# Performance work log

Measured on AMD Instinct MI355X. Metric: run time of the kernel, lower is better.

Reference implementation:

```python
import jax, jax.numpy as jnp
import numpy as np

B = 8; C = 128; EXP = 4; H = 112; W = 112; K = 3; PAD = 1; STRIDE = 1
IN_C = C * EXP  # 512
EPS = 1e-5


def setup_inputs() -> dict:
    key = jax.random.key(0)
    ks = jax.random.split(key, 24)
    f32 = jnp.float32

    def n(k, shape, s=0.05):
        return jax.random.normal(k, shape, f32) * s

    def bn_params(k):
        k1, k2, k3, k4 = jax.random.split(k, 4)
        g = 1.0 + 0.1 * jax.random.normal(k1, (), f32)  # placeholder, per-channel below
        return k1, k2, k3, k4

    inp = {}
    inp["x"] = jax.random.normal(ks[0], (B, IN_C, H, W), f32)
    # conv1: 1x1, 512 -> 128
    inp["w1"] = n(ks[1], (C, IN_C))
    inp["b1"] = n(ks[2], (C,))
    # bn1
    inp["g1"] = 1.0 + 0.1 * jax.random.normal(ks[3], (C,), f32)
    inp["be1"] = 0.1 * jax.random.normal(ks[4], (C,), f32)
    inp["m1"] = 0.1 * jax.random.normal(ks[5], (C,), f32)
    inp["v1"] = 1.0 + 0.1 * jax.random.uniform(ks[6], (C,), f32)
    # offset conv: 3x3, C -> 18 (small weights so sampling offsets stay modest)
    inp["woff"] = n(ks[7], (2 * K * K, C, K, K), 0.01)
    inp["boff"] = jnp.zeros((2 * K * K,), f32)
    # deformable conv weight: 3x3, C -> C
    inp["wd"] = n(ks[8], (C, C, K, K))
    inp["bd"] = n(ks[9], (C,))
    # bn2
    inp["g2"] = 1.0 + 0.1 * jax.random.normal(ks[10], (C,), f32)
    inp["be2"] = 0.1 * jax.random.normal(ks[11], (C,), f32)
    inp["m2"] = 0.1 * jax.random.normal(ks[12], (C,), f32)
    inp["v2"] = 1.0 + 0.1 * jax.random.uniform(ks[13], (C,), f32)
    # conv2: 1x1, 128 -> 512
    inp["w2"] = n(ks[14], (IN_C, C))
    inp["b2"] = n(ks[15], (IN_C,))
    # bn3
    inp["g3"] = 1.0 + 0.1 * jax.random.normal(ks[16], (IN_C,), f32)
    inp["be3"] = 0.1 * jax.random.normal(ks[17], (IN_C,), f32)
    inp["m3"] = 0.1 * jax.random.normal(ks[18], (IN_C,), f32)
    inp["v3"] = 1.0 + 0.1 * jax.random.uniform(ks[19], (IN_C,), f32)
    return inp


def conv1x1(x, w, b):
    return jnp.einsum("oc,bchw->bohw", w, x) + b[None, :, None, None]


def bn(x, g, be, m, v):
    inv = g / jnp.sqrt(v + EPS)
    return x * inv[None, :, None, None] + (be - m * inv)[None, :, None, None]


def conv3x3(x, w, b):
    out = jax.lax.conv_general_dilated(
        x, w, (STRIDE, STRIDE), ((PAD, PAD), (PAD, PAD)),
        dimension_numbers=("NCHW", "OIHW", "NCHW"))
    return out + b[None, :, None, None]


def deform_conv(x, offset, w, b):
    # x: [B, Cin, H, W]; offset: [B, 2*K*K, Ho, Wo] (y,x interleaved per kernel pt)
    Bn, Cin, Hh, Ww = x.shape
    Ho, Wo = offset.shape[2], offset.shape[3]
    P = Ho * Wo
    off = offset.reshape(Bn, K * K, 2, Ho, Wo)
    kk = jnp.arange(K * K)
    ky = (kk // K).astype(jnp.float32)  # 0..2
    kx = (kk % K).astype(jnp.float32)
    base_y = jnp.arange(Ho, dtype=jnp.float32) * STRIDE - PAD
    base_x = jnp.arange(Wo, dtype=jnp.float32) * STRIDE - PAD
    py = base_y[None, None, :, None] + ky[None, :, None, None] + off[:, :, 0]  # [B,9,Ho,Wo]
    px = base_x[None, None, None, :] + kx[None, :, None, None] + off[:, :, 1]
    y0 = jnp.floor(py); x0 = jnp.floor(px)
    dy = (py - y0).reshape(Bn, 1, -1)  # [B,1,9*P]
    dx = (px - x0).reshape(Bn, 1, -1)
    x_flat = x.reshape(Bn, Cin, Hh * Ww)

    def gather(yi, xi):
        valid = ((yi >= 0) & (yi <= Hh - 1) & (xi >= 0) & (xi <= Ww - 1))
        yc = jnp.clip(yi, 0, Hh - 1).astype(jnp.int32)
        xc = jnp.clip(xi, 0, Ww - 1).astype(jnp.int32)
        idx = (yc * Ww + xc).reshape(Bn, -1)  # [B, 9*P]
        g = jax.vmap(lambda xb, ib: xb[:, ib])(x_flat, idx)  # [B, Cin, 9*P]
        return g * valid.reshape(Bn, 1, -1).astype(x.dtype)

    v00 = gather(y0, x0)
    v01 = gather(y0, x0 + 1)
    v10 = gather(y0 + 1, x0)
    v11 = gather(y0 + 1, x0 + 1)
    cols = (v00 * (1 - dy) * (1 - dx) + v01 * (1 - dy) * dx
            + v10 * dy * (1 - dx) + v11 * dy * dx)  # [B, Cin, 9*P]
    cols = cols.reshape(Bn, Cin * K * K, P)
    out = jnp.einsum("oi,bip->bop", w.reshape(w.shape[0], -1), cols)
    out = out + b[None, :, None]
    return out.reshape(Bn, w.shape[0], Ho, Wo)


def reference(x, w1, b1, g1, be1, m1, v1, woff, boff, wd, bd,
              g2, be2, m2, v2, w2, b2, g3, be3, m3, v3):
    out = jax.nn.relu(bn(conv1x1(x, w1, b1), g1, be1, m1, v1))
    offset = conv3x3(out, woff, boff)
    out = deform_conv(out, offset, wd, bd)
    out = bn(out, g2, be2, m2, v2)
    out = bn(conv1x1(out, w2, b2), g3, be3, m3, v3)
    return jax.nn.relu(out + x)
```

## Files before the change

### kernel.cpp

```cpp
#include <hip/hip_runtime.h>
#include <hip/hip_bf16.h>


typedef __attribute__((ext_vector_type(8))) short short8;
typedef __attribute__((ext_vector_type(4))) float f32x4;

constexpr int Bn = 8;
constexpr int IC = 512;
constexpr int Cc = 128;
constexpr int Hh = 112;
constexpr int Ww = 112;
constexpr int Pp = Hh * Ww;
constexpr float EPSf = 1e-5f;

constexpr size_t OFS_OFFS  = 0;
constexpr size_t OFS_OUT2B = 2097152;
constexpr size_t OFS_W1B   = (size_t)Bn * Pp * IC / 2;
constexpr size_t OFS_W2B   = OFS_W1B + (size_t)Cc * IC / 2;
constexpr size_t OFS_WDB   = OFS_W2B + (size_t)IC * Cc / 2;
constexpr size_t OFS_WOFB  = OFS_WDB + (size_t)9 * Cc * Cc / 2;

__device__ __forceinline__ ushort f2bf(float f) {
  uint u = __float_as_uint(f);
  return (ushort)((u + 0x7fffu + ((u >> 16) & 1u)) >> 16);
}
__device__ __forceinline__ float bfLO(uint u) {
  return __uint_as_float(u << 16);
}
__device__ __forceinline__ float bfHI(uint u) {
  return __uint_as_float(u & 0xffff0000u);
}
__device__ __forceinline__ uint cvtpk(float a, float b) {
  __hip_bfloat162 h = __float22bfloat162_rn(make_float2(a, b));
  return *(uint*)&h;
}

__global__ __launch_bounds__(256) void prep_kernel(
    const float* __restrict__ w1, const float* __restrict__ w2,
    const float* __restrict__ wd, const float* __restrict__ woff,
    float* __restrict__ ws) {
  ushort* w1b  = (ushort*)(ws + OFS_W1B);
  ushort* w2b  = (ushort*)(ws + OFS_W2B);
  ushort* wdb  = (ushort*)(ws + OFS_WDB);
  ushort* wofb = (ushort*)(ws + OFS_WOFB);
  const int n1 = Cc * IC;
  const int n2 = IC * Cc;
  const int n3 = 9 * Cc * Cc;
  const int n4 = 9 * 32 * Cc;
  const int total = n1 + n2 + n3 + n4;
  for (int idx = blockIdx.x * blockDim.x + threadIdx.x; idx < total;
       idx += gridDim.x * blockDim.x) {
    if (idx < n1) {
      w1b[idx] = f2bf(w1[idx]);
    } else if (idx < n1 + n2) {
      int t = idx - n1;
      w2b[t] = f2bf(w2[t]);
    } else if (idx < n1 + n2 + n3) {
      int t = idx - n1 - n2;
      int k = t / (Cc * Cc), r = t % (Cc * Cc);
      int oc = r / Cc, ic = r % Cc;
      wdb[t] = f2bf(wd[(oc * Cc + ic) * 9 + k]);
    } else {
      int t = idx - n1 - n2 - n3;
      int k = t / (32 * Cc), r = t % (32 * Cc);
      int oc = r / Cc, ic = r % Cc;
      wofb[t] = (oc < 18) ? f2bf(woff[(oc * Cc + ic) * 9 + k]) : (ushort)0;
    }
  }
}

__global__ __launch_bounds__(256) void k1_fused_mfma(
    const float* __restrict__ x, const ushort* __restrict__ w1b,
    const float* __restrict__ b1, const float* __restrict__ g1,
    const float* __restrict__ be1, const float* __restrict__ m1,
    const float* __restrict__ v1, ushort* __restrict__ out1b) {
  __shared__ ushort smem[26624];

  const int tid = threadIdx.x;
  const int lane = tid & 63;
  const int wv = tid >> 6;
  const int lr = lane & 15, lg = lane >> 4;
  const int orig = blockIdx.x;
  const int bid = (orig & 7) * 98 + (orig >> 3);
  const int bi = bid / 98;
  const int pblk = (bid % 98) * 128;

  float xs[2][4][2][2];
  short8 wsv[2][2];

#define BAR_LGKM asm volatile("s_waitcnt lgkmcnt(0)\ns_barrier" ::: "memory")

#define LOADX(c, s)                                                       \
  {                                                                       \
    const float* xb_ = x + ((size_t)bi * IC + (size_t)((c) * 32 + wv * 8)) * Pp \
                         + pblk + lane;                                   \
    _Pragma("unroll") for (int q = 0; q < 4; ++q) {                       \
      _Pragma("unroll") for (int p = 0; p < 2; ++p) {                     \
        xs[s][q][p][0] = xb_[(size_t)(2 * q + p) * Pp];                   \
        xs[s][q][p][1] = xb_[(size_t)(2 * q + p) * Pp + 64];              \
      }                                                                   \
    }                                                                     \
  }

#define LOADW(c, s)                                                       \
  {                                                                       \
    const ushort* wb_ = w1b + (size_t)(wv * 32 + (lane >> 2)) * IC        \
                            + (c) * 32 + (lane & 3) * 8;                  \
    wsv[s][0] = *(const short8*)(wb_);                                    \
    wsv[s][1] = *(const short8*)(wb_ + (size_t)16 * IC);                  \
  }

#define WRITE(c, s)                                                       \
  {                                                                       \
    char* atb_ = (char*)smem + ((c) & 1) * 16384;                         \
    _Pragma("unroll") for (int e = 0; e < 2; ++e) {                       \
      const int px_ = lane + 64 * e;                                      \
      uint4 pk_;                                                          \
      uint* pp_ = (uint*)&pk_;                                            \
      _Pragma("unroll") for (int q = 0; q < 4; ++q)                       \
        pp_[q] = cvtpk(xs[s][q][0][e], xs[s][q][1][e]);                   \
      *(uint4*)(atb_ + px_ * 128 + ((wv ^ (px_ & 7)) << 4)) = pk_;        \
    }                                                                     \
    ushort* wlb_ = smem + 16384 + ((c) & 1) * 5120;                       \
    *(short8*)(wlb_ + (wv * 32 + (lane >> 2)) * 40 + (lane & 3) * 8) = wsv[s][0]; \
    *(short8*)(wlb_ + (wv * 32 + 16 + (lane >> 2)) * 40 + (lane & 3) * 8) = wsv[s][1]; \
  }

  f32x4 acc[2][8];
#pragma unroll
  for (int m = 0; m < 2; ++m)
#pragma unroll
    for (int n = 0; n < 8; ++n) acc[m][n] = (f32x4)0.f;

  LOADX(0, 0) LOADW(0, 0)
  LOADX(1, 1) LOADW(1, 1)

#pragma unroll
  for (int c = 0; c < 16; ++c) {
    WRITE(c, c & 1);
    BAR_LGKM;
    if (c + 2 < 16) { LOADX(c + 2, c & 1) LOADW(c + 2, c & 1) }

    {
      const char* atb = (const char*)smem + (c & 1) * 16384;
      const ushort* wlb = smem + 16384 + (c & 1) * 5120;
      const int sw = (lg ^ (lr & 7)) << 4;
      short8 a0 = *(const short8*)(atb + (wv * 32 + lr) * 128 + sw);
      short8 a1 = *(const short8*)(atb + (wv * 32 + 16 + lr) * 128 + sw);
#pragma unroll
      for (int n = 0; n < 8; ++n) {
        short8 b = *(const short8*)(wlb + (n * 16 + lr) * 40 + lg * 8);
        acc[0][n] = __builtin_amdgcn_mfma_f32_16x16x32_bf16(a0, b, acc[0][n], 0, 0, 0);
        acc[1][n] = __builtin_amdgcn_mfma_f32_16x16x32_bf16(a1, b, acc[1][n], 0, 0, 0);
      }
    }
  }

#undef LOADX
#undef LOADW
#undef WRITE
#undef BAR_LGKM

  __syncthreads();

  ushort(*Ab)[136] = (ushort(*)[136])smem;
#pragma unroll
  for (int n = 0; n < 8; ++n) {
    int oc = n * 16 + lr;
    float inv = g1[oc] * rsqrtf(v1[oc] + EPSf);
    float sh = (b1[oc] - m1[oc]) * inv + be1[oc];
#pragma unroll
    for (int m = 0; m < 2; ++m) {
#pragma unroll
      for (int r = 0; r < 4; ++r) {
        int pl = wv * 32 + m * 16 + lg * 4 + r;
        Ab[pl][oc] = f2bf(fmaxf(acc[m][n][r] * inv + sh, 0.f));
      }
    }
  }
#pragma unroll
  for (int j = 0; j < 8; ++j) {
    int pl = wv * 32 + j * 4 + (lane >> 4);
    uint4 v = *(const uint4*)&Ab[pl][(lane & 15) * 8];
    *(uint4*)(out1b + ((size_t)bi * Pp + pblk + pl) * Cc + (lane & 15) * 8) = v;
  }
}

__global__ __launch_bounds__(256) void k2_offset_mfma(
    const ushort* __restrict__ out1b, const ushort* __restrict__ wofb,
    const float* __restrict__ boff, float* __restrict__ offs) {
  const int tid = threadIdx.x;
  const int lane = tid & 63;
  const int wv = tid >> 6;
  const int lr = lane & 15, lg = lane >> 4;
  const int orig = blockIdx.x;
  const int bid = (orig & 7) * 49 + (orig >> 3);
  const int bi = bid / 49;
  const int p0 = (bid % 49) * 256 + wv * 64;

  const ushort* src = out1b + (size_t)bi * Pp * Cc;

  int ohm[4], owm[4];
#pragma unroll
  for (int m = 0; m < 4; ++m) {
    int p = p0 + m * 16 + lr;
    ohm[m] = p / Ww;
    owm[m] = p - ohm[m] * Ww;
  }

  f32x4 acc[4][2];
#pragma unroll
  for (int m = 0; m < 4; ++m) { acc[m][0] = (f32x4)0.f; acc[m][1] = (f32x4)0.f; }

  for (int k = 0; k < 9; ++k) {
    const int kdy = k / 3 - 1, kdx = k % 3 - 1;
    const ushort* rp[4];
    bool val[4];
#pragma unroll
    for (int m = 0; m < 4; ++m) {
      int yy = ohm[m] + kdy, xx = owm[m] + kdx;
      val[m] = ((unsigned)yy < (unsigned)Hh) && ((unsigned)xx < (unsigned)Ww);
      int yc = min(max(yy, 0), Hh - 1), xc = min(max(xx, 0), Ww - 1);
      rp[m] = src + (size_t)(yc * Ww + xc) * Cc;
    }
#pragma unroll
    for (int ks = 0; ks < 4; ++ks) {
      short8 b0 = *(const short8*)(wofb + (size_t)(k * 32 + lr) * Cc + ks * 32 + 8 * lg);
      short8 b1v = *(const short8*)(wofb + (size_t)(k * 32 + 16 + lr) * Cc + ks * 32 + 8 * lg);
#pragma unroll
      for (int m = 0; m < 4; ++m) {
        short8 av = *(const short8*)(rp[m] + ks * 32 + 8 * lg);
        short8 a = val[m] ? av : (short8)0;
        acc[m][0] = __builtin_amdgcn_mfma_f32_16x16x32_bf16(a, b0, acc[m][0], 0, 0, 0);
        acc[m][1] = __builtin_amdgcn_mfma_f32_16x16x32_bf16(a, b1v, acc[m][1], 0, 0, 0);
      }
    }
  }

#pragma unroll
  for (int n = 0; n < 2; ++n) {
    int oc = n * 16 + lr;
    if (oc < 18) {
      float bo = boff[oc];
      float* orow = offs + ((size_t)bi * 18 + oc) * Pp;
#pragma unroll
      for (int m = 0; m < 4; ++m) {
        int p = p0 + m * 16 + lg * 4;
        float4 o;
        o.x = acc[m][n][0] + bo;
        o.y = acc[m][n][1] + bo;
        o.z = acc[m][n][2] + bo;
        o.w = acc[m][n][3] + bo;
        *(float4*)(orow + p) = o;
      }
    }
  }
}

__global__ __launch_bounds__(256) void k3_deform_mfma(
    const ushort* __restrict__ out1b, const float* __restrict__ offs,
    const ushort* __restrict__ wdb, const float* __restrict__ bd,
    const float* __restrict__ g2, const float* __restrict__ be2,
    const float* __restrict__ m2, const float* __restrict__ v2,
    ushort* __restrict__ out2b) {
  __shared__ ushort colsA[2][64][136];
  __shared__ float meta[9 * 64 * 8];

  const int tid = threadIdx.x;
  const int lane = tid & 63;
  const int wv = tid >> 6;
  const int lr = lane & 15, lg = lane >> 4;
  const int orig = blockIdx.x;
  const int bid = (orig & 7) * 196 + (orig >> 3);
  const int bi = bid / 196;
  const int p0 = (bid % 196) * 64;

  const ushort* src = out1b + (size_t)bi * Pp * Cc;
  const float* offb = offs + (size_t)bi * 18 * Pp;

  {
    const int p = p0 + lane;
    const int oh = p / Ww, ow = p - oh * Ww;
    for (int k = wv; k < 9; k += 4) {
      const int kdy = k / 3 - 1, kdx = k % 3 - 1;
      float py = (float)(oh + kdy) + offb[(size_t)(2 * k) * Pp + p];
      float pxf = (float)(ow + kdx) + offb[(size_t)(2 * k + 1) * Pp + p];
      float y0f = floorf(py), x0f = floorf(pxf);
      float dy = py - y0f, dx = pxf - x0f;
      int y0 = (int)y0f, x0 = (int)x0f;
      int y1 = y0 + 1, x1 = x0 + 1;
      float wy0 = (y0 >= 0 && y0 < Hh) ? 1.f - dy : 0.f;
      float wy1 = (y1 >= 0 && y1 < Hh) ? dy : 0.f;
      float wx0 = (x0 >= 0 && x0 < Ww) ? 1.f - dx : 0.f;
      float wx1 = (x1 >= 0 && x1 < Ww) ? dx : 0.f;
      int yc0 = min(max(y0, 0), Hh - 1), yc1 = min(max(y1, 0), Hh - 1);
      int xc0 = min(max(x0, 0), Ww - 1), xc1 = min(max(x1, 0), Ww - 1);
      float* mp = &meta[(k * 64 + lane) * 8];
      mp[0] = wy0 * wx0;
      mp[1] = wy0 * wx1;
      mp[2] = wy1 * wx0;
      mp[3] = wy1 * wx1;
      int* ip = (int*)(mp + 4);
      ip[0] = (yc0 * Ww + xc0) * (Cc * 2);
      ip[1] = (yc0 * Ww + xc1) * (Cc * 2);
      ip[2] = (yc1 * Ww + xc0) * (Cc * 2);
      ip[3] = (yc1 * Ww + xc1) * (Cc * 2);
    }
  }
  __syncthreads();

  f32x4 acc[4][2];
#pragma unroll
  for (int m = 0; m < 4; ++m) { acc[m][0] = (f32x4)0.f; acc[m][1] = (f32x4)0.f; }

  const int pxq = lane >> 4;
  const int l16 = lane & 15;
  const char* sb = (const char*)src + l16 * 16;

  uint4 gv[4][4];
  float4 gw[4];

#define BAR_LGKM asm volatile("s_waitcnt lgkmcnt(0)\ns_barrier" ::: "memory")

#define ISSUE(kk, t)                                                     \
  {                                                                      \
    const int px_ = wv * 16 + (t) * 4 + pxq;                             \
    const float* mp_ = &meta[((kk) * 64 + px_) * 8];                     \
    gw[t] = *(const float4*)mp_;                                         \
    int4 o4_ = *(const int4*)(mp_ + 4);                                  \
    gv[t][0] = *(const uint4*)(sb + o4_.x);                              \
    gv[t][1] = *(const uint4*)(sb + o4_.y);                              \
    gv[t][2] = *(const uint4*)(sb + o4_.z);                              \
    gv[t][3] = *(const uint4*)(sb + o4_.w);                              \
  }

#define COMMIT(buf, t)                                                   \
  {                                                                      \
    const int px_ = wv * 16 + (t) * 4 + pxq;                             \
    float4 w4_ = gw[t];                                                  \
    uint4 pk_;                                                           \
    uint* pkp_ = (uint*)&pk_;                                            \
    _Pragma("unroll")                                                    \
    for (int j = 0; j < 4; ++j) {                                        \
      uint a0_ = ((const uint*)&gv[t][0])[j];                            \
      uint a1_ = ((const uint*)&gv[t][1])[j];                            \
      uint a2_ = ((const uint*)&gv[t][2])[j];                            \
      uint a3_ = ((const uint*)&gv[t][3])[j];                            \
      float lo_ = w4_.x * bfLO(a0_) + w4_.y * bfLO(a1_)                  \
                + w4_.z * bfLO(a2_) + w4_.w * bfLO(a3_);                 \
      float hi_ = w4_.x * bfHI(a0_) + w4_.y * bfHI(a1_)                  \
                + w4_.z * bfHI(a2_) + w4_.w * bfHI(a3_);                 \
      pkp_[j] = cvtpk(lo_, hi_);                                         \
    }                                                                    \
    *(uint4*)&colsA[buf][px_][l16 * 8] = pk_;                            \
  }

  ISSUE(0, 0) ISSUE(0, 1) ISSUE(0, 2) ISSUE(0, 3)
  COMMIT(0, 0) COMMIT(0, 1) COMMIT(0, 2) COMMIT(0, 3)
  ISSUE(1, 0) ISSUE(1, 1) ISSUE(1, 2) ISSUE(1, 3)
  BAR_LGKM;

  for (int k = 0; k < 9; ++k) {
    const int cur = k & 1;
    const int nxt = cur ^ 1;
    const ushort* wk = wdb + (size_t)k * Cc * Cc + (size_t)(wv * 32) * Cc;

#pragma unroll
    for (int ks = 0; ks < 4; ++ks) {
      short8 b0 = *(const short8*)(wk + lr * Cc + ks * 32 + 8 * lg);
      short8 b1v = *(const short8*)(wk + (16 + lr) * Cc + ks * 32 + 8 * lg);
#pragma unroll
      for (int m = 0; m < 4; ++m) {
        short8 a = *(const short8*)&colsA[cur][m * 16 + lr][ks * 32 + 8 * lg];
        acc[m][0] = __builtin_amdgcn_mfma_f32_16x16x32_bf16(a, b0, acc[m][0], 0, 0, 0);
        acc[m][1] = __builtin_amdgcn_mfma_f32_16x16x32_bf16(a, b1v, acc[m][1], 0, 0, 0);
      }
    }

    if (k < 8) {
      COMMIT(nxt, 0)
      if (k < 7) { ISSUE(k + 2, 0) }
      COMMIT(nxt, 1)
      if (k < 7) { ISSUE(k + 2, 1) }
      COMMIT(nxt, 2)
      if (k < 7) { ISSUE(k + 2, 2) }
      COMMIT(nxt, 3)
      if (k < 7) { ISSUE(k + 2, 3) }
      BAR_LGKM;
    }
  }

#undef ISSUE
#undef COMMIT
#undef BAR_LGKM

#pragma unroll
  for (int n = 0; n < 2; ++n) {
    int oc = wv * 32 + n * 16 + lr;
    float inv = g2[oc] * rsqrtf(v2[oc] + EPSf);
    float sh = (bd[oc] - m2[oc]) * inv + be2[oc];
#pragma unroll
    for (int m = 0; m < 4; ++m) {
#pragma unroll
      for (int r = 0; r < 4; ++r) {
        int p = p0 + m * 16 + lg * 4 + r;
        out2b[((size_t)bi * Pp + p) * Cc + oc] = f2bf(acc[m][n][r] * inv + sh);
      }
    }
  }
}

__global__ __launch_bounds__(256, 2) void k4_mfma(
    const ushort* __restrict__ out2b, const ushort* __restrict__ w2b,
    const float* __restrict__ b2, const float* __restrict__ g3,
    const float* __restrict__ be3, const float* __restrict__ m3,
    const float* __restrict__ v3, const float* __restrict__ x,
    float* __restrict__ out) {
  __shared__ float obuf[2][16][260];

  const int tid = threadIdx.x;
  const int lane = tid & 63;
  const int wv = tid >> 6;
  const int lr = lane & 15, lg = lane >> 4;
  const int orig = blockIdx.x;
  const int bid = (orig & 7) * 392 + (orig >> 3);
  const int bi = bid / 392;
  const int r392 = bid % 392;
  const int oc_t = r392 / 49;
  const int pblk = (r392 % 49) * 256;
  const int p0 = pblk + wv * 64;
  const int ocb = oc_t * 64;

  const ushort* A = out2b + ((size_t)bi * Pp + p0) * Cc;
  const ushort* Bw = w2b + (size_t)ocb * Cc;

  float4 xv[4][4];
#pragma unroll
  for (int n = 0; n < 4; ++n)
#pragma unroll
    for (int it = 0; it < 4; ++it) {
      int oc = ocb + n * 16 + it * 4 + wv;
      xv[n][it] = *(const float4*)(x + ((size_t)bi * IC + oc) * Pp + pblk + lane * 4);
    }

  f32x4 acc[4][4];
#pragma unroll
  for (int m = 0; m < 4; ++m)
#pragma unroll
    for (int n = 0; n < 4; ++n) acc[m][n] = (f32x4)0.f;

#pragma unroll
  for (int ks = 0; ks < 4; ++ks) {
    short8 a[4];
#pragma unroll
    for (int m = 0; m < 4; ++m)
      a[m] = *(const short8*)(A + (size_t)(m * 16 + lr) * Cc + ks * 32 + 8 * lg);
#pragma unroll
    for (int n = 0; n < 4; ++n) {
      short8 b = *(const short8*)(Bw + (size_t)(n * 16 + lr) * Cc + ks * 32 + 8 * lg);
#pragma unroll
      for (int m = 0; m < 4; ++m)
        acc[m][n] = __builtin_amdgcn_mfma_f32_16x16x32_bf16(a[m], b, acc[m][n], 0, 0, 0);
    }
  }

#pragma unroll
  for (int n = 0; n < 4; ++n) {
    {
      int ocw = ocb + n * 16 + lr;
      float inv = g3[ocw] * rsqrtf(v3[ocw] + EPSf);
      float sh = (b2[ocw] - m3[ocw]) * inv + be3[ocw];
      float(*buf)[260] = obuf[n & 1];
#pragma unroll
      for (int m = 0; m < 4; ++m) {
        float4 o;
        o.x = acc[m][n][0] * inv + sh;
        o.y = acc[m][n][1] * inv + sh;
        o.z = acc[m][n][2] * inv + sh;
        o.w = acc[m][n][3] * inv + sh;
        *(float4*)&buf[lr][wv * 64 + m * 16 + lg * 4] = o;
      }
    }
    __syncthreads();
    {
      const float(*buf)[260] = obuf[n & 1];
#pragma unroll
      for (int it = 0; it < 4; ++it) {
        int r = it * 4 + wv;
        int oc = ocb + n * 16 + r;
        float4 v = *(const float4*)&buf[r][lane * 4];
        float4 xr = xv[n][it];
        float4 o;
        o.x = fmaxf(v.x + xr.x, 0.f);
        o.y = fmaxf(v.y + xr.y, 0.f);
        o.z = fmaxf(v.z + xr.z, 0.f);
        o.w = fmaxf(v.w + xr.w, 0.f);
        *(float4*)(out + ((size_t)bi * IC + oc) * Pp + pblk + lane * 4) = o;
      }
    }
  }
}

extern "C" void kernel_launch(void* const* d_in, const int* in_sizes, int n_in,
                              void* d_out, int out_size, void* d_ws, size_t ws_size,
                              hipStream_t stream) {
  const float* x    = (const float*)d_in[0];
  const float* w1   = (const float*)d_in[1];
  const float* b1   = (const float*)d_in[2];
  const float* g1   = (const float*)d_in[3];
  const float* be1  = (const float*)d_in[4];
  const float* m1   = (const float*)d_in[5];
  const float* v1   = (const float*)d_in[6];
  const float* woff = (const float*)d_in[7];
  const float* boff = (const float*)d_in[8];
  const float* wd   = (const float*)d_in[9];
  const float* bd   = (const float*)d_in[10];
  const float* g2   = (const float*)d_in[11];
  const float* be2  = (const float*)d_in[12];
  const float* m2   = (const float*)d_in[13];
  const float* v2   = (const float*)d_in[14];
  const float* w2   = (const float*)d_in[15];
  const float* b2   = (const float*)d_in[16];
  const float* g3   = (const float*)d_in[17];
  const float* be3  = (const float*)d_in[18];
  const float* m3   = (const float*)d_in[19];
  const float* v3   = (const float*)d_in[20];

  float* ws   = (float*)d_ws;
  float* out  = (float*)d_out;
  float*  offs  = ws + OFS_OFFS;
  ushort* out2b = (ushort*)(ws + OFS_OUT2B);
  ushort* w1b   = (ushort*)(ws + OFS_W1B);
  ushort* w2b   = (ushort*)(ws + OFS_W2B);
  ushort* wdb   = (ushort*)(ws + OFS_WDB);
  ushort* wofb  = (ushort*)(ws + OFS_WOFB);
  ushort* out1b = (ushort*)d_out;

  prep_kernel<<<512, 256, 0, stream>>>(w1, w2, wd, woff, ws);
  k1_fused_mfma<<<Bn * 98, 256, 0, stream>>>(x, w1b, b1, g1, be1, m1, v1, out1b);
  k2_offset_mfma<<<Bn * 49, 256, 0, stream>>>(out1b, wofb, boff, offs);
  k3_deform_mfma<<<Bn * 196, 256, 0, stream>>>(out1b, offs, wdb, bd,
                                               g2, be2, m2, v2, out2b);
  k4_mfma<<<Bn * 392, 256, 0, stream>>>(out2b, w2b, b2, g3, be3, m3, v3, x, out);
}
```

Baseline: 313.8 us.

## Fuse offset convolution into deformable conv kernel via shared-memory partial sums

Removes the separate offset-conv kernel and computes the 18-channel offset 3x3 conv inside the deform kernel. Each wave handles a subset of the 9 taps for the block's 64 pixels, stores partial sums in the shared colsA buffer, and the sums are reduced together with the bias when the sampling metadata is built. This drops a kernel launch and the fp32 offset tensor's write and read through global memory. In exchange it adds MFMA work and a barrier before the deform stage, and reuses the colsA shared memory, which must not overlap with later uses.

```diff
diff --git a/kernel.cpp b/kernel.cpp
--- a/kernel.cpp
+++ b/kernel.cpp
@@ -186,79 +186,9 @@
   }
 }
 
-__global__ __launch_bounds__(256) void k2_offset_mfma(
+__global__ __launch_bounds__(256) void k3_deform_mfma(
     const ushort* __restrict__ out1b, const ushort* __restrict__ wofb,
-    const float* __restrict__ boff, float* __restrict__ offs) {
-  const int tid = threadIdx.x;
-  const int lane = tid & 63;
-  const int wv = tid >> 6;
-  const int lr = lane & 15, lg = lane >> 4;
-  const int orig = blockIdx.x;
-  const int bid = (orig & 7) * 49 + (orig >> 3);
-  const int bi = bid / 49;
-  const int p0 = (bid % 49) * 256 + wv * 64;
-
-  const ushort* src = out1b + (size_t)bi * Pp * Cc;
-
-  int ohm[4], owm[4];
-#pragma unroll
-  for (int m = 0; m < 4; ++m) {
-    int p = p0 + m * 16 + lr;
-    ohm[m] = p / Ww;
-    owm[m] = p - ohm[m] * Ww;
-  }
-
-  f32x4 acc[4][2];
-#pragma unroll
-  for (int m = 0; m < 4; ++m) { acc[m][0] = (f32x4)0.f; acc[m][1] = (f32x4)0.f; }
-
-  for (int k = 0; k < 9; ++k) {
-    const int kdy = k / 3 - 1, kdx = k % 3 - 1;
-    const ushort* rp[4];
-    bool val[4];
-#pragma unroll
-    for (int m = 0; m < 4; ++m) {
-      int yy = ohm[m] + kdy, xx = owm[m] + kdx;
-      val[m] = ((unsigned)yy < (unsigned)Hh) && ((unsigned)xx < (unsigned)Ww);
-      int yc = min(max(yy, 0), Hh - 1), xc = min(max(xx, 0), Ww - 1);
-      rp[m] = src + (size_t)(yc * Ww + xc) * Cc;
-    }
-#pragma unroll
-    for (int ks = 0; ks < 4; ++ks) {
-      short8 b0 = *(const short8*)(wofb + (size_t)(k * 32 + lr) * Cc + ks * 32 + 8 * lg);
-      short8 b1v = *(const short8*)(wofb + (size_t)(k * 32 + 16 + lr) * Cc + ks * 32 + 8 * lg);
-#pragma unroll
-      for (int m = 0; m < 4; ++m) {
-        short8 av = *(const short8*)(rp[m] + ks * 32 + 8 * lg);
-        short8 a = val[m] ? av : (short8)0;
-        acc[m][0] = __builtin_amdgcn_mfma_f32_16x16x32_bf16(a, b0, acc[m][0], 0, 0, 0);
-        acc[m][1] = __builtin_amdgcn_mfma_f32_16x16x32_bf16(a, b1v, acc[m][1], 0, 0, 0);
-      }
-    }
-  }
-
-#pragma unroll
-  for (int n = 0; n < 2; ++n) {
-    int oc = n * 16 + lr;
-    if (oc < 18) {
-      float bo = boff[oc];
-      float* orow = offs + ((size_t)bi * 18 + oc) * Pp;
-#pragma unroll
-      for (int m = 0; m < 4; ++m) {
-        int p = p0 + m * 16 + lg * 4;
-        float4 o;
-        o.x = acc[m][n][0] + bo;
-        o.y = acc[m][n][1] + bo;
-        o.z = acc[m][n][2] + bo;
-        o.w = acc[m][n][3] + bo;
-        *(float4*)(orow + p) = o;
-      }
-    }
-  }
-}
-
-__global__ __launch_bounds__(256) void k3_deform_mfma(
-    const ushort* __restrict__ out1b, const float* __restrict__ offs,
+    const float* __restrict__ boff,
     const ushort* __restrict__ wdb, const float* __restrict__ bd,
     const float* __restrict__ g2, const float* __restrict__ be2,
     const float* __restrict__ m2, const float* __restrict__ v2,
@@ -276,15 +206,69 @@
   const int p0 = (bid % 196) * 64;
 
   const ushort* src = out1b + (size_t)bi * Pp * Cc;
-  const float* offb = offs + (size_t)bi * 18 * Pp;
+  float* pacc = (float*)colsA;
+
+  {
+    int ohm[4], owm[4];
+#pragma unroll
+    for (int m = 0; m < 4; ++m) {
+      int p = p0 + m * 16 + lr;
+      ohm[m] = p / Ww;
+      owm[m] = p - ohm[m] * Ww;
+    }
+    f32x4 aco[4][2];
+#pragma unroll
+    for (int m = 0; m < 4; ++m) { aco[m][0] = (f32x4)0.f; aco[m][1] = (f32x4)0.f; }
+
+    for (int k = wv; k < 9; k += 4) {
+      const int kdy = k / 3 - 1, kdx = k % 3 - 1;
+      const ushort* rp[4];
+      bool val[4];
+#pragma unroll
+      for (int m = 0; m < 4; ++m) {
+        int yy = ohm[m] + kdy, xx = owm[m] + kdx;
+        val[m] = ((unsigned)yy < (unsigned)Hh) && ((unsigned)xx < (unsigned)Ww);
+        int yc = min(max(yy, 0), Hh - 1), xc = min(max(xx, 0), Ww - 1);
+        rp[m] = src + (size_t)(yc * Ww + xc) * Cc;
+      }
+#pragma unroll
+      for (int ks = 0; ks < 4; ++ks) {
+        short8 b0 = *(const short8*)(wofb + (size_t)(k * 32 + lr) * Cc + ks * 32 + 8 * lg);
+        short8 b1v = *(const short8*)(wofb + (size_t)(k * 32 + 16 + lr) * Cc + ks * 32 + 8 * lg);
+#pragma unroll
+        for (int m = 0; m < 4; ++m) {
+          short8 av = *(const short8*)(rp[m] + ks * 32 + 8 * lg);
+          short8 a = val[m] ? av : (short8)0;
+          aco[m][0] = __builtin_amdgcn_mfma_f32_16x16x32_bf16(a, b0, aco[m][0], 0, 0, 0);
+          aco[m][1] = __builtin_amdgcn_mfma_f32_16x16x32_bf16(a, b1v, aco[m][1], 0, 0, 0);
+        }
+      }
+    }
+#pragma unroll
+    for (int n = 0; n < 2; ++n)
+#pragma unroll
+      for (int m = 0; m < 4; ++m)
+#pragma unroll
+        for (int r = 0; r < 4; ++r) {
+          int px = m * 16 + lg * 4 + r;
+          pacc[(wv * 64 + px) * 33 + n * 16 + lr] = aco[m][n][r];
+        }
+  }
+  __syncthreads();
 
   {
     const int p = p0 + lane;
     const int oh = p / Ww, ow = p - oh * Ww;
     for (int k = wv; k < 9; k += 4) {
       const int kdy = k / 3 - 1, kdx = k % 3 - 1;
-      float py = (float)(oh + kdy) + offb[(size_t)(2 * k) * Pp + p];
-      float pxf = (float)(ow + kdx) + offb[(size_t)(2 * k + 1) * Pp + p];
+      float offy = boff[2 * k], offx = boff[2 * k + 1];
+#pragma unroll
+      for (int w = 0; w < 4; ++w) {
+        offy += pacc[(w * 64 + lane) * 33 + 2 * k];
+        offx += pacc[(w * 64 + lane) * 33 + 2 * k + 1];
+      }
+      float py = (float)(oh + kdy) + offy;
+      float pxf = (float)(ow + kdx) + offx;
       float y0f = floorf(py), x0f = floorf(pxf);
       float dy = py - y0f, dx = pxf - x0f;
       int y0 = (int)y0f, x0 = (int)x0f;
@@ -528,7 +512,6 @@
 
   float* ws   = (float*)d_ws;
   float* out  = (float*)d_out;
-  float*  offs  = ws + OFS_OFFS;
   ushort* out2b = (ushort*)(ws + OFS_OUT2B);
   ushort* w1b   = (ushort*)(ws + OFS_W1B);
   ushort* w2b   = (ushort*)(ws + OFS_W2B);
@@ -538,8 +521,7 @@
 
   prep_kernel<<<512, 256, 0, stream>>>(w1, w2, wd, woff, ws);
   k1_fused_mfma<<<Bn * 98, 256, 0, stream>>>(x, w1b, b1, g1, be1, m1, v1, out1b);
-  k2_offset_mfma<<<Bn * 49, 256, 0, stream>>>(out1b, wofb, boff, offs);
-  k3_deform_mfma<<<Bn * 196, 256, 0, stream>>>(out1b, offs, wdb, bd,
+  k3_deform_mfma<<<Bn * 196, 256, 0, stream>>>(out1b, wofb, boff, wdb, bd,
                                                g2, be2, m2, v2, out2b);
   k4_mfma<<<Bn * 392, 256, 0, stream>>>(out2b, w2b, b2, g3, be3, m3, v3, x, out);
 }
```

After: 311.5 us. About the same (-0.7%).
